# Optimization experiments

Measured on AMD Instinct MI355X. Metric: run time of the kernel, lower is better.

## Reference

```python
import jax, jax.numpy as jnp
import numpy as np

NUM_CLASSES = 11
LOW_T, HIGH_T, EPS = 0.1, 0.2, 1e-6
_DN = ('NCHW', 'OIHW', 'NCHW')

# 5-tap Gaussian (kornia Canny defaults: kernel_size=(5,5), sigma=(1,1))
_g = np.exp(-(np.arange(5.0) - 2.0) ** 2 / 2.0); _g /= _g.sum()
GAUSS_1D = jnp.asarray(_g, dtype=jnp.float32)
# Sobel kernels (unnormalized, as used inside kornia Canny): (2,1,3,3) = [gx, gy]
SOBEL = jnp.asarray(np.stack([
    [[-1.0, 0.0, 1.0], [-2.0, 0.0, 2.0], [-1.0, 0.0, 1.0]],
    [[-1.0, -2.0, -1.0], [0.0, 0.0, 0.0], [1.0, 2.0, 1.0]],
])[:, None], dtype=jnp.float32)
# kornia get_canny_nms_kernel: 8 directional (center=+1, neighbor=-1) kernels
_nms = np.zeros((8, 1, 3, 3), np.float32)
_offs = [(1, 2), (0, 2), (0, 1), (0, 0), (1, 0), (2, 0), (2, 1), (2, 2)]
for _i, (_r, _c) in enumerate(_offs):
    _nms[_i, 0, 1, 1] = 1.0
    _nms[_i, 0, _r, _c] = -1.0
NMS_K = jnp.asarray(_nms)
# hysteresis: "any 8-neighbor is strong" == conv with ring-of-ones > 0
_ring = np.ones((1, 1, 3, 3), np.float32); _ring[0, 0, 1, 1] = 0.0
RING_K = jnp.asarray(_ring)


def _conv(x, k, pad):
    return jax.lax.conv_general_dilated(x, k, (1, 1), pad, dimension_numbers=_DN)


def gaussian_blur(x):  # reflect border, separable 5x5
    xp = jnp.pad(x, ((0, 0), (0, 0), (2, 2), (2, 2)), mode='reflect')
    xp = _conv(xp, GAUSS_1D.reshape(1, 1, 5, 1), 'VALID')
    return _conv(xp, GAUSS_1D.reshape(1, 1, 1, 5), 'VALID')


def canny_edges(x):  # x: (N,1,H,W) -> binary thin edges (N,1,H,W), kornia Canny()[1]
    b = gaussian_blur(x)
    bp = jnp.pad(b, ((0, 0), (0, 0), (1, 1), (1, 1)), mode='edge')  # replicate pad
    g = _conv(bp, SOBEL, 'VALID')                 # (N,2,H,W)
    gx, gy = g[:, :1], g[:, 1:]
    mag = jnp.sqrt(gx * gx + gy * gy + EPS)
    ang = jnp.round(jnp.rad2deg(jnp.arctan2(gy, gx)) / 45.0)  # units of 45 deg
    nms = _conv(mag, NMS_K, 'SAME')               # (N,8,H,W)
    pos = jnp.mod(ang, 8.0).astype(jnp.int32)
    neg = jnp.mod(ang + 4.0, 8.0).astype(jnp.int32)
    cp = jnp.take_along_axis(nms, pos, axis=1)
    cn = jnp.take_along_axis(nms, neg, axis=1)
    mag = mag * (jnp.minimum(cp, cn) > 0.0)       # non-max suppression
    edges = (mag > LOW_T) * 0.5 + (mag > HIGH_T) * 0.5  # 0 / weak(0.5) / strong(1)

    def hyst_step(e):
        weak = (e == 0.5).astype(e.dtype)
        strong = (e == 1.0).astype(e.dtype)
        conn = (_conv(strong, RING_K, 'SAME') > 0).astype(e.dtype)
        hyst = conn * weak + strong
        return hyst + (hyst == 0) * weak * 0.5, hyst

    def cond(st):
        return jnp.any(st[0] != st[1])

    def body(st):
        new, _ = hyst_step(st[0])
        return (new, st[0])

    e_fin, _ = jax.lax.while_loop(cond, body, (edges, -jnp.ones_like(edges)))
    return hyst_step(e_fin)[1]  # final binary hysteresis map


def dilate_cross(x):  # kornia dilation with cross kernel, geodesic border (x >= 0)
    xp = jnp.pad(x, ((0, 0), (0, 0), (1, 1), (1, 1)))
    c = xp[:, :, 1:-1, 1:-1]
    up, dn = xp[:, :, :-2, 1:-1], xp[:, :, 2:, 1:-1]
    lf, rt = xp[:, :, 1:-1, :-2], xp[:, :, 1:-1, 2:]
    return jnp.maximum(jnp.maximum(jnp.maximum(c, up), jnp.maximum(dn, lf)), rt)


def boundary_target(gt):
    onehot = (gt[:, None, :, :] == jnp.arange(NUM_CLASSES)[None, :, None, None]).astype(jnp.float32)
    B, C, H, W = onehot.shape
    e = canny_edges(onehot.reshape(B * C, 1, H, W))  # vectorized over the 11-channel loop
    edge_gt = dilate_cross(e).reshape(B, C, H, W)
    return onehot, edge_gt


def setup_inputs() -> dict:
    key = jax.random.key(0)
    k1, k2, k3 = jax.random.split(key, 3)
    pd = jax.random.normal(k1, (8, 11, 512, 512), dtype=jnp.float32)
    gt = jax.random.randint(k2, (8, 512, 512), 0, 11)
    weight = jax.random.uniform(k3, (11,), dtype=jnp.float32)
    return {"pd": pd, "gt": gt, "weight": weight}


def reference(pd, gt, weight):
    onehot, edge_gt = boundary_target(gt)
    pd_prob = jax.nn.log_softmax(pd, axis=1)
    boundary_gt = onehot + 2.0 * edge_gt * onehot
    return -(weight * jnp.sum(pd_prob * boundary_gt, axis=(0, 2, 3))).sum() / onehot.sum()
```

## Files before the change

### kernel.cpp

```cpp
#include <hip/hip_runtime.h>
#include <cstdint>
#include <cmath>

#define HH 512
#define WW 512
#define NB 8
#define NC 11
#define NPIX (HH*WW)
#define NWPR 8
#define NWORDS (HH*NWPR)
#define NL2B 256

typedef unsigned long long u64;
typedef uint32_t u32;
typedef unsigned short u16;

__device__ __forceinline__ int reflect512(int t) {
  t = t < 0 ? -t : t;
  return t > 511 ? 1022 - t : t;
}

__device__ __forceinline__ float h2f(u16 h) {
  _Float16 v = __builtin_bit_cast(_Float16, h);
  return (float)v;
}
__device__ __forceinline__ u16 f2h(float f) {
  _Float16 v = (_Float16)f;
  return __builtin_bit_cast(u16, v);
}

__global__ __launch_bounds__(256) void k_onehot(const int* __restrict__ gt,
                                                u64* __restrict__ planes) {
  int wave = (blockIdx.x * 256 + threadIdx.x) >> 6;
  int lane = threadIdx.x & 63;
  for (int j = wave; j < NB*512*8; j += 4096) {
    int img = j >> 12;
    int rw = j & 4095;
    int gv = gt[(size_t)img*NPIX + rw*64 + lane];
    u64 my = 0;
    #pragma unroll
    for (int c = 0; c < NC; ++c) {
      u64 m = __ballot(gv == c);
      if (lane == c) my = m;
    }
    if (lane < NC)
      planes[(size_t)img*NC*NWORDS + (size_t)lane*NWORDS + rw] = my;
  }
}

#define TA 64

__global__ __launch_bounds__(256) void k_edges_lse(const u64* __restrict__ planes,
                                                   u64* __restrict__ strongw,
                                                   u64* __restrict__ weakw,
                                                   const float* __restrict__ pd,
                                                   const int* __restrict__ gt,
                                                   const float* __restrict__ wt,
                                                   float* __restrict__ tbuf,
                                                   double* __restrict__ acc) {
  __shared__ u64 sbits[72][2];
  __shared__ u16 sbh[68*68];
  __shared__ u16 su[68*72];
  __shared__ float red[4];
  __shared__ u16 slut[32];

  const int tid = threadIdx.x;
  const int bid = blockIdx.x;
  const int grpi = bid / 15;
  const int role = bid - grpi*15;

  if (role >= 11) {
    int j = grpi*4 + (role - 11);
    int t = j * 256 + tid;
    int b = t >> 16;
    int p = (t & 65535) * 4;
    int4 g4 = *(const int4*)(gt + (size_t)b*NPIX + p);
    const float* pb = pd + (size_t)b * NC * NPIX + p;
    float s0=0.f,s1=0.f,s2=0.f,s3=0.f;
    float v0=0.f,v1=0.f,v2=0.f,v3=0.f;
    #pragma unroll
    for (int c = 0; c < NC; ++c) {
      float4 x = *(const float4*)(pb + (size_t)c * NPIX);
      if (c == g4.x) v0 = x.x;
      if (c == g4.y) v1 = x.y;
      if (c == g4.z) v2 = x.z;
      if (c == g4.w) v3 = x.w;
      s0 += __expf(x.x);
      s1 += __expf(x.y);
      s2 += __expf(x.z);
      s3 += __expf(x.w);
    }
    float4 o;
    o.x = wt[g4.x] * (v0 - __logf(s0));
    o.y = wt[g4.y] * (v1 - __logf(s1));
    o.z = wt[g4.z] * (v2 - __logf(s2));
    o.w = wt[g4.w] * (v3 - __logf(s3));
    *(float4*)(tbuf + (size_t)b*NPIX + p) = o;
    float s = o.x + o.y + o.z + o.w;
    #pragma unroll
    for (int off = 32; off > 0; off >>= 1) s += __shfl_down(s, off, 64);
    if ((tid & 63) == 0) red[tid >> 6] = s;
    __syncthreads();
    if (tid == 0) {
      double d = (double)red[0] + (double)red[1] + (double)red[2] + (double)red[3];
      atomicAdd(acc, d);
    }
    return;
  }

  const int e = grpi*11 + role;
  const int z = e >> 6;
  const int rem = e & 63;
  const int r0 = (rem >> 3) * TA, c0 = (rem & 7) * TA;
  const u64* plane = planes + (size_t)z * NWORDS;

  const float g0 = 0.054488684549642945f;
  const float g1 = 0.24420134200323332f;
  const float g2 = 0.4026199468942475f;

  if (tid < 32) {
    float v = ((tid & 1) ? g0 : 0.f) + ((tid & 2) ? g1 : 0.f) + ((tid & 4) ? g2 : 0.f)
            + ((tid & 8) ? g1 : 0.f) + ((tid & 16) ? g0 : 0.f);
    slut[tid] = f2h(v);
  }

  if (tid < 72) {
    int gr = reflect512(r0 + tid - 4);
    const u64* prow = plane + gr*8;
    int wi = c0 >> 6;
    u64 b = prow[wi];
    u64 w0, w1;
    if (c0 == 0) {
      u64 cc = prow[1];
      w0 = (b << 4) | ((__brevll(b) >> 59) & 0xFull);
      w1 = (b >> 60) | (cc << 4);
    } else if (c0 == WW - TA) {
      u64 a = prow[wi-1];
      w0 = (a >> 60) | (b << 4);
      w1 = (b >> 60) | (((__brevll(b) >> 1) & 0xFull) << 4);
    } else {
      u64 a = prow[wi-1];
      u64 cc = prow[wi+1];
      w0 = (a >> 60) | (b << 4);
      w1 = (b >> 60) | (cc << 4);
    }
    sbits[tid][0] = w0;
    sbits[tid][1] = w1;
  }
  __syncthreads();

  u16* t1h = su;
  {
    int grp = tid % 18, row = tid / 18;
    for (int k = 0; k < 5; ++k) {
      if (row < 68) {
        int widx = grp >> 4;
        int shift = (grp & 15) * 4;
        u32 idx4 = 0;
        #pragma unroll
        for (int d = 0; d < 5; ++d) {
          u32 nib = (u32)(sbits[row+d][widx] >> shift) & 0xFu;
          u32 sp = (nib * 0x00204081u) & 0x01010101u;
          idx4 |= sp << d;
        }
        ushort4 o;
        o.x = slut[idx4 & 31u];
        o.y = slut[(idx4 >> 8) & 31u];
        o.z = slut[(idx4 >> 16) & 31u];
        o.w = slut[idx4 >> 24];
        *(ushort4*)&t1h[row*72 + grp*4] = o;
      }
      grp += 4; row += 14;
      if (grp >= 18) { grp -= 18; row += 1; }
    }
  }
  __syncthreads();

  {
    int grp = tid % 17, row = tid / 17;
    for (int k = 0; k < 5; ++k) {
      if (row < 68) {
        const u16* rp = &t1h[row*72 + grp*4];
        ushort4 ua = *(const ushort4*)rp;
        ushort4 ub = *(const ushort4*)(rp + 4);
        float a0=h2f(ua.x), a1=h2f(ua.y), a2=h2f(ua.z), a3=h2f(ua.w);
        float b0=h2f(ub.x), b1=h2f(ub.y), b2=h2f(ub.z), b3=h2f(ub.w);
        ushort4 o;
        o.x = f2h(g0*(a0 + b0) + g1*(a1 + a3) + g2*a2);
        o.y = f2h(g0*(a1 + b1) + g1*(a2 + b0) + g2*a3);
        o.z = f2h(g0*(a2 + b2) + g1*(a3 + b1) + g2*b0);
        o.w = f2h(g0*(a3 + b3) + g1*(b0 + b2) + g2*b1);
        *(ushort4*)&sbh[row*68 + grp*4] = o;
      }
      grp += 1; row += 15;
      if (grp >= 17) { grp -= 17; row += 1; }
    }
  }
  __syncthreads();

  {
    const bool rb0 = (r0 == 0), rb1 = (r0 == HH-TA);
    const bool cb0 = (c0 == 0), cb1 = (c0 == WW-TA);
    if (rb0 | rb1 | cb0 | cb1) {
      for (int i = tid; i < 528; i += 256) {
        int rr, cc;
        if (i < 272) {
          int rI = i / 68;
          rr = (rI < 2) ? rI : 64 + rI;
          cc = i - rI*68;
        } else {
          int j = i - 272;
          rr = 2 + (j >> 2);
          int cI = j & 3;
          cc = (cI < 2) ? cI : 64 + cI;
        }
        int sr = (rb0 && rr < 2) ? 2 : ((rb1 && rr > 65) ? 65 : rr);
        int sc = (cb0 && cc < 2) ? 2 : ((cb1 && cc > 65) ? 65 : cc);
        if (sr != rr || sc != cc) sbh[rr*68 + cc] = sbh[sr*68 + sc];
      }
      __syncthreads();
    }
  }

  u16* mgh = su;
  for (int k = 0; k < 5; ++k) {
    int idx = tid + 256*k;
    if (idx < 66*16) {
      int row = idx >> 4;
      int g = idx & 15;
      int cbase = g*4;
      const u16* p0 = &sbh[row*68 + cbase];
      ushort4 a0 = *(const ushort4*)(p0);
      ushort2 b0 = *(const ushort2*)(p0 + 4);
      ushort4 a1 = *(const ushort4*)(p0 + 68);
      ushort2 b1 = *(const ushort2*)(p0 + 72);
      ushort4 a2 = *(const ushort4*)(p0 + 136);
      ushort2 b2 = *(const ushort2*)(p0 + 140);
      float ur[6], vr[6];
      {
        float t0, t1v, t2;
        t0 = h2f(a0.x); t1v = h2f(a1.x); t2 = h2f(a2.x);
        ur[0] = t0 + 2.f*t1v + t2;  vr[0] = t2 - t0;
        t0 = h2f(a0.y); t1v = h2f(a1.y); t2 = h2f(a2.y);
        ur[1] = t0 + 2.f*t1v + t2;  vr[1] = t2 - t0;
        t0 = h2f(a0.z); t1v = h2f(a1.z); t2 = h2f(a2.z);
        ur[2] = t0 + 2.f*t1v + t2;  vr[2] = t2 - t0;
        t0 = h2f(a0.w); t1v = h2f(a1.w); t2 = h2f(a2.w);
        ur[3] = t0 + 2.f*t1v + t2;  vr[3] = t2 - t0;
        t0 = h2f(b0.x); t1v = h2f(b1.x); t2 = h2f(b2.x);
        ur[4] = t0 + 2.f*t1v + t2;  vr[4] = t2 - t0;
        t0 = h2f(b0.y); t1v = h2f(b1.y); t2 = h2f(b2.y);
        ur[5] = t0 + 2.f*t1v + t2;  vr[5] = t2 - t0;
      }
      int gm = r0 + row - 1;
      ushort4 ov;
      u16* ovp = &ov.x;
      #pragma unroll
      for (int jj = 0; jj < 4; ++jj) {
        float gx = ur[jj+2] - ur[jj];
        float gy = vr[jj] + 2.f*vr[jj+1] + vr[jj+2];
        float gx2 = gx*gx, gy2 = gy*gy;
        float mvf = gx2 + gy2;
        int axis;
        if (gy2 <= 0.17157287525f*gx2) axis = 0;
        else if (gy2 >= 5.82842712475f*gx2) axis = 2;
        else axis = (gx*gy > 0.f) ? 1 : 3;
        int gmc = c0 + cbase + jj - 1;
        u16 bits = (u16)((f2h(mvf) & 0xFFFCu) | (u16)axis);
        bool in = ((unsigned)gm < 512u) && ((unsigned)gmc < 512u);
        ovp[jj] = in ? bits : (u16)0;
      }
      *(ushort4*)&mgh[row*68 + cbase] = ov;
    }
  }
  if (tid < 132) {
    int row = tid >> 1, col = 64 + (tid & 1);
    const u16* p0 = &sbh[row*68 + col];
    float b00=h2f(p0[0]),   b01=h2f(p0[1]),   b02=h2f(p0[2]);
    float b10=h2f(p0[68]),                     b12=h2f(p0[70]);
    float b20=h2f(p0[136]), b21=h2f(p0[137]), b22=h2f(p0[138]);
    float gx = (b02 + 2.f*b12 + b22) - (b00 + 2.f*b10 + b20);
    float gy = (b20 + 2.f*b21 + b22) - (b00 + 2.f*b01 + b02);
    float gx2 = gx*gx, gy2 = gy*gy;
    float mvf = gx2 + gy2;
    int axis;
    if (gy2 <= 0.17157287525f*gx2) axis = 0;
    else if (gy2 >= 5.82842712475f*gx2) axis = 2;
    else axis = (gx*gy > 0.f) ? 1 : 3;
    int gm = r0 + row - 1, gmc = c0 + col - 1;
    u16 bits = (u16)((f2h(mvf) & 0xFFFCu) | (u16)axis);
    bool in = ((unsigned)gm < 512u) && ((unsigned)gmc < 512u);
    mgh[row*68 + col] = in ? bits : (u16)0;
  }
  __syncthreads();

  const int lane = tid & 63;
  const int wv = tid >> 6;
  const u32 THS = (u32)(f2h(0.039999f) & 0xFFFCu);
  const u32 THW = (u32)(f2h(0.009999f) & 0xFFFCu);
  size_t obase = (size_t)z * NWORDS + (size_t)r0*NWPR + (size_t)(c0 >> 6);
  for (int k = 0; k < 16; ++k) {
    int lr = wv + k*4;
    u32 mw = mgh[(lr+1)*68 + (lane+1)];
    u32 m = mw & 0xFFFCu;
    int a = mw & 3;
    int dr = ((0x01 >> (2*a)) & 3) - 1;
    int dc = ((0x1A >> (2*a)) & 3) - 1;
    u32 m1 = mgh[(lr+1+dr)*68 + (lane+1+dc)] & 0xFFFCu;
    u32 m2 = mgh[(lr+1-dr)*68 + (lane+1-dc)] & 0xFFFCu;
    bool pass = (m > m1) && (m > m2);
    u64 sw = __ballot(pass && m > THS);
    u64 wk = __ballot(pass && m > THW);
    if (lane == 0) {
      strongw[obase + (size_t)lr*NWPR] = sw;
      weakw  [obase + (size_t)lr*NWPR] = wk;
    }
  }
}

__global__ __launch_bounds__(512) void k_hyst(const u64* __restrict__ strongw,
                                              const u64* __restrict__ weakw,
                                              const u64* __restrict__ planes,
                                              u64* __restrict__ dc) {
  __shared__ u64 btop[8][8];
  __shared__ u64 bbot[8][8];
  __shared__ int gflag;
  const int z = blockIdx.x;
  const int tid = threadIdx.x;
  const int lane = tid & 63;
  const int w = tid >> 6;
  const int row = tid;

  const u64* sg = strongw + (size_t)z * NWORDS + (size_t)row * NWPR;
  const u64* wg = weakw   + (size_t)z * NWORDS + (size_t)row * NWPR;

  u64 S[8], W[8], Wr[8];
  #pragma unroll
  for (int cw = 0; cw < 8; ++cw) { S[cw] = sg[cw]; W[cw] = wg[cw]; Wr[cw] = __brevll(W[cw]); }

  if (tid == 0) gflag = 0;
  if (lane == 0) {
    #pragma unroll
    for (int cw = 0; cw < 8; ++cw) btop[w][cw] = S[cw];
  }
  if (lane == 63) {
    #pragma unroll
    for (int cw = 0; cw < 8; ++cw) bbot[w][cw] = S[cw];
  }
  __syncthreads();

  for (int outer = 0; outer < 200; ++outer) {
    u64 up_b[8], dn_b[8];
    #pragma unroll
    for (int cw = 0; cw < 8; ++cw) {
      up_b[cw] = (w > 0) ? bbot[w-1][cw] : 0ull;
      dn_b[cw] = (w < 7) ? btop[w+1][cw] : 0ull;
    }
    int wchg = 0;
    for (int inner = 0; inner < 256; ++inner) {
      u64 v[8], changed = 0;
      #pragma unroll
      for (int cw = 0; cw < 8; ++cw) {
        u64 up = __shfl_up(S[cw], 1, 64);
        if (lane == 0) up = up_b[cw];
        u64 dn = __shfl_down(S[cw], 1, 64);
        if (lane == 63) dn = dn_b[cw];
        v[cw] = up | S[cw] | dn;
      }
      #pragma unroll
      for (int cw = 0; cw < 8; ++cw) {
        u64 vp = (cw > 0) ? v[cw-1] : 0ull;
        u64 vn = (cw < 7) ? v[cw+1] : 0ull;
        u64 D = (v[cw] << 1) | v[cw] | (v[cw] >> 1) | (vp >> 63) | (vn << 63);
        u64 seeds = W[cw] & D;
        u64 L = W[cw] & ~(W[cw] + seeds);
        u64 sr = __brevll(seeds);
        u64 R = __brevll(Wr[cw] & ~(Wr[cw] + sr));
        u64 ns = S[cw] | seeds | L | R;
        changed |= ns ^ S[cw];
        S[cw] = ns;
      }
      if (!__any(changed != 0ull)) break;
      wchg = 1;
    }
    if (wchg && lane == 0) gflag = 1;
    __syncthreads();
    if (lane == 0) {
      #pragma unroll
      for (int cw = 0; cw < 8; ++cw) btop[w][cw] = S[cw];
    }
    if (lane == 63) {
      #pragma unroll
      for (int cw = 0; cw < 8; ++cw) bbot[w][cw] = S[cw];
    }
    int f = gflag;
    __syncthreads();
    if (tid == 0) gflag = 0;
    __syncthreads();
    if (!f) break;
  }

  u64 d[8];
  #pragma unroll
  for (int cw = 0; cw < 8; ++cw) {
    u64 up = __shfl_up(S[cw], 1, 64);
    if (lane == 0) up = (w > 0) ? bbot[w-1][cw] : 0ull;
    u64 dn = __shfl_down(S[cw], 1, 64);
    if (lane == 63) dn = (w < 7) ? btop[w+1][cw] : 0ull;
    d[cw] = S[cw] | (S[cw] << 1) | (S[cw] >> 1) | up | dn;
  }
  #pragma unroll
  for (int cw = 0; cw < 8; ++cw) {
    if (cw > 0) d[cw] |= S[cw-1] >> 63;
    if (cw < 7) d[cw] |= S[cw+1] << 63;
  }

  const u64* prow = planes + (size_t)z * NWORDS + (size_t)row * NWPR;
  u64* dgc = dc + (size_t)z * NWORDS + (size_t)row * NWPR;
  #pragma unroll
  for (int cw = 0; cw < 8; cw += 2) {
    ulonglong2 v2;
    v2.x = d[cw]   & prow[cw];
    v2.y = d[cw+1] & prow[cw+1];
    *(ulonglong2*)&dgc[cw] = v2;
  }
}

__global__ __launch_bounds__(256) void k_loss2(const float* __restrict__ tbuf,
                                               const u32* __restrict__ dc32,
                                               double* __restrict__ acc,
                                               double* __restrict__ acc2,
                                               unsigned int* __restrict__ cnt,
                                               float* __restrict__ out) {
  int t = blockIdx.x * 256 + threadIdx.x;
  int img = t >> 13;
  int wi = t & 8191;
  u32 m = 0;
  #pragma unroll
  for (int c = 0; c < NC; ++c)
    m |= dc32[((size_t)(img*NC + c) << 13) + wi];
  const float* tb = tbuf + ((size_t)img << 18) + ((size_t)wi << 5);
  float s = 0.f;
  #pragma unroll
  for (int q = 0; q < 8; ++q) {
    float4 x = *(const float4*)(tb + q*4);
    if ((m >> (q*4))     & 1u) s += x.x;
    if ((m >> (q*4 + 1)) & 1u) s += x.y;
    if ((m >> (q*4 + 2)) & 1u) s += x.z;
    if ((m >> (q*4 + 3)) & 1u) s += x.w;
  }
  #pragma unroll
  for (int o = 32; o > 0; o >>= 1) s += __shfl_down(s, o, 64);
  __shared__ float wsum[4];
  if ((threadIdx.x & 63) == 0) wsum[threadIdx.x >> 6] = s;
  __syncthreads();
  if (threadIdx.x == 0) {
    double d = (double)wsum[0] + (double)wsum[1] + (double)wsum[2] + (double)wsum[3];
    atomicAdd(acc2, d);
    __threadfence();
    unsigned int old = atomicAdd(cnt, 1u);
    if (old == NL2B - 1) {
      double t1 = atomicAdd(acc, 0.0);
      double t2 = atomicAdd(acc2, 0.0);
      out[0] = (float)(-(t1 + 2.0*t2) / 2097152.0);
    }
  }
}

extern "C" void kernel_launch(void* const* d_in, const int* in_sizes, int n_in,
                              void* d_out, int out_size, void* d_ws, size_t ws_size,
                              hipStream_t stream) {
  const float* pd = (const float*)d_in[0];
  const int*   gt = (const int*)d_in[1];
  const float* wt = (const float*)d_in[2];
  float* out = (float*)d_out;

  double* acc  = (double*)d_ws;
  double* acc2 = (double*)((char*)d_ws + 8);
  unsigned int* cnt = (unsigned int*)((char*)d_ws + 16);
  u64* planes  = (u64*)((char*)d_ws + 256);
  u64* strongw = planes  + (size_t)NB*NC*NWORDS;
  u64* weakw   = strongw + (size_t)NB*NC*NWORDS;
  u64* dc      = weakw   + (size_t)NB*NC*NWORDS;
  float* tbuf  = (float*)(dc + (size_t)NB*NC*NWORDS);

  (void)hipMemsetAsync(d_ws, 0, 256, stream);

  k_onehot<<<1024, 256, 0, stream>>>(gt, planes);

  k_edges_lse<<<512*15, 256, 0, stream>>>(planes, strongw, weakw, pd, gt, wt, tbuf, acc);

  k_hyst<<<NB*NC, 512, 0, stream>>>(strongw, weakw, planes, dc);

  k_loss2<<<NL2B, 256, 0, stream>>>(tbuf, (const u32*)dc, acc, acc2, cnt, out);
}
```

Measured before the change: 103.1 us.

## Fuse final loss reduction into hysteresis kernel via last-block-per-image tail

After: 191.3 us. 85.6% more time.

```diff
diff --git a/kernel.cpp b/kernel.cpp
--- a/kernel.cpp
+++ b/kernel.cpp
@@ -9,7 +9,6 @@
 #define NPIX (HH*WW)
 #define NWPR 8
 #define NWORDS (HH*NWPR)
-#define NL2B 256
 
 typedef unsigned long long u64;
 typedef uint32_t u32;
@@ -19,7 +18,6 @@
   t = t < 0 ? -t : t;
   return t > 511 ? 1022 - t : t;
 }
-
 __device__ __forceinline__ float h2f(u16 h) {
   _Float16 v = __builtin_bit_cast(_Float16, h);
   return (float)v;
@@ -321,15 +319,24 @@
 __global__ __launch_bounds__(512) void k_hyst(const u64* __restrict__ strongw,
                                               const u64* __restrict__ weakw,
                                               const u64* __restrict__ planes,
-                                              u64* __restrict__ dc) {
+                                              u64* __restrict__ dc,
+                                              const float* __restrict__ tbuf,
+                                              double* __restrict__ acc,
+                                              double* __restrict__ acc2,
+                                              u32* __restrict__ cnt,
+                                              u32* __restrict__ hcnt,
+                                              float* __restrict__ out) {
   __shared__ u64 btop[8][8];
   __shared__ u64 bbot[8][8];
+  __shared__ float fred[8];
   __shared__ int gflag;
+  __shared__ int lastflag;
   const int z = blockIdx.x;
   const int tid = threadIdx.x;
   const int lane = tid & 63;
   const int w = tid >> 6;
   const int row = tid;
+  const int img = z / NC;
 
   const u64* sg = strongw + (size_t)z * NWORDS + (size_t)row * NWPR;
   const u64* wg = weakw   + (size_t)z * NWORDS + (size_t)row * NWPR;
@@ -424,42 +431,45 @@
     v2.y = d[cw+1] & prow[cw+1];
     *(ulonglong2*)&dgc[cw] = v2;
   }
-}
-
-__global__ __launch_bounds__(256) void k_loss2(const float* __restrict__ tbuf,
-                                               const u32* __restrict__ dc32,
-                                               double* __restrict__ acc,
-                                               double* __restrict__ acc2,
-                                               unsigned int* __restrict__ cnt,
-                                               float* __restrict__ out) {
-  int t = blockIdx.x * 256 + threadIdx.x;
-  int img = t >> 13;
-  int wi = t & 8191;
-  u32 m = 0;
-  #pragma unroll
-  for (int c = 0; c < NC; ++c)
-    m |= dc32[((size_t)(img*NC + c) << 13) + wi];
-  const float* tb = tbuf + ((size_t)img << 18) + ((size_t)wi << 5);
+
+  __threadfence();
+  __syncthreads();
+  if (tid == 0) lastflag = (atomicAdd(&hcnt[img], 1u) == (u32)(NC - 1)) ? 1 : 0;
+  __syncthreads();
+  if (!lastflag) return;
+  __threadfence();
+
+  const u32* dc32 = (const u32*)dc;
   float s = 0.f;
   #pragma unroll
-  for (int q = 0; q < 8; ++q) {
-    float4 x = *(const float4*)(tb + q*4);
-    if ((m >> (q*4))     & 1u) s += x.x;
-    if ((m >> (q*4 + 1)) & 1u) s += x.y;
-    if ((m >> (q*4 + 2)) & 1u) s += x.z;
-    if ((m >> (q*4 + 3)) & 1u) s += x.w;
+  for (int k = 0; k < 16; ++k) {
+    int wi = tid + (k << 9);
+    u32 m = 0;
+    #pragma unroll
+    for (int c = 0; c < NC; ++c)
+      m |= dc32[((size_t)(img*NC + c) << 13) + wi];
+    const float* tb = tbuf + ((size_t)img << 18) + ((size_t)wi << 5);
+    #pragma unroll
+    for (int q = 0; q < 8; ++q) {
+      float4 x = *(const float4*)(tb + q*4);
+      if ((m >> (q*4))     & 1u) s += x.x;
+      if ((m >> (q*4 + 1)) & 1u) s += x.y;
+      if ((m >> (q*4 + 2)) & 1u) s += x.z;
+      if ((m >> (q*4 + 3)) & 1u) s += x.w;
+    }
   }
   #pragma unroll
   for (int o = 32; o > 0; o >>= 1) s += __shfl_down(s, o, 64);
-  __shared__ float wsum[4];
-  if ((threadIdx.x & 63) == 0) wsum[threadIdx.x >> 6] = s;
-  __syncthreads();
-  if (threadIdx.x == 0) {
-    double d = (double)wsum[0] + (double)wsum[1] + (double)wsum[2] + (double)wsum[3];
-    atomicAdd(acc2, d);
+  if (lane == 0) fred[w] = s;
+  __syncthreads();
+  if (tid == 0) {
+    double dsum = 0.0;
+    #pragma unroll
+    for (int i = 0; i < 8; ++i) dsum += (double)fred[i];
+    atomicAdd(acc2, dsum);
     __threadfence();
-    unsigned int old = atomicAdd(cnt, 1u);
-    if (old == NL2B - 1) {
+    u32 old = atomicAdd(cnt, 1u);
+    if (old == (u32)(NB - 1)) {
       double t1 = atomicAdd(acc, 0.0);
       double t2 = atomicAdd(acc2, 0.0);
       out[0] = (float)(-(t1 + 2.0*t2) / 2097152.0);
@@ -475,10 +485,12 @@
   const float* wt = (const float*)d_in[2];
   float* out = (float*)d_out;
 
-  double* acc  = (double*)d_ws;
-  double* acc2 = (double*)((char*)d_ws + 8);
-  unsigned int* cnt = (unsigned int*)((char*)d_ws + 16);
-  u64* planes  = (u64*)((char*)d_ws + 256);
+  char* base = (char*)d_ws;
+  double* acc  = (double*)base;
+  double* acc2 = (double*)(base + 8);
+  u32* cnt  = (u32*)(base + 16);
+  u32* hcnt = (u32*)(base + 32);
+  u64* planes  = (u64*)(base + 256);
   u64* strongw = planes  + (size_t)NB*NC*NWORDS;
   u64* weakw   = strongw + (size_t)NB*NC*NWORDS;
   u64* dc      = weakw   + (size_t)NB*NC*NWORDS;
@@ -490,7 +502,5 @@
 
   k_edges_lse<<<512*15, 256, 0, stream>>>(planes, strongw, weakw, pd, gt, wt, tbuf, acc);
 
-  k_hyst<<<NB*NC, 512, 0, stream>>>(strongw, weakw, planes, dc);
-
-  k_loss2<<<NL2B, 256, 0, stream>>>(tbuf, (const u32*)dc, acc, acc2, cnt, out);
-}
+  k_hyst<<<NB*NC, 512, 0, stream>>>(strongw, weakw, planes, dc, tbuf, acc, acc2, cnt, hcnt, out);
+}
```
